# Optimization experiments

Hardware: AMD Instinct MI355X
Metric: run time of the kernel (lower is better)

## Reference

```python
import jax, jax.numpy as jnp
from jax import lax
import numpy as np

D_MODEL = 1024
D_STATE = 16
D_CONV = 4
EXPAND = 2
D_INNER = EXPAND * D_MODEL  # 2048
DT_RANK = D_MODEL // 16     # 64
BATCH = 2
SEQLEN = 1024


def setup_inputs() -> dict:
    key = jax.random.key(0)
    ks = iter(jax.random.split(key, 32))

    def nrm(shape, s=0.02):
        return jax.random.normal(next(ks), shape, jnp.float32) * s

    def mamba_params():
        return dict(
            Win=nrm((2 * D_INNER, D_MODEL)), bin=jnp.zeros((2 * D_INNER,), jnp.float32),
            convw=nrm((D_INNER, D_CONV), 0.1), convb=jnp.zeros((D_INNER,), jnp.float32),
            Wx=nrm((DT_RANK + 2 * D_STATE, D_INNER)),
            Wdt=nrm((D_INNER, DT_RANK), 0.1), bdt=nrm((D_INNER,), 0.1),
            Alog=jnp.log(jnp.broadcast_to(jnp.arange(1, D_STATE + 1, dtype=jnp.float32), (D_INNER, D_STATE))),
            Dsk=jnp.ones((D_INNER,), jnp.float32),
            Wout=nrm((D_MODEL, D_INNER)), bout=jnp.zeros((D_MODEL,), jnp.float32),
        )

    inp = {"x": jax.random.normal(next(ks), (BATCH, SEQLEN, D_MODEL), jnp.float32)}
    for pref, p in (("f_", mamba_params()), ("b_", mamba_params())):
        for k, v in p.items():
            inp[pref + k] = v
    inp["proj_W"] = nrm((D_MODEL, 2 * D_MODEL))
    inp["proj_b"] = jnp.zeros((D_MODEL,), jnp.float32)
    return inp


def selective_scan(u, delta, A, Bm, Cm, Dsk):
    # u, delta: (B,L,Di); Bm, Cm: (B,L,N); A: (Di,N); Dsk: (Di,)
    def step(h, inp):
        u_t, d_t, b_t, c_t = inp  # (B,Di),(B,Di),(B,N),(B,N)
        dA = jnp.exp(d_t[..., None] * A)                      # (B,Di,N)
        h = h * dA + (d_t * u_t)[..., None] * b_t[:, None, :]  # (B,Di,N)
        y = jnp.einsum('bdn,bn->bd', h, c_t)
        return h, y

    h0 = jnp.zeros((u.shape[0], A.shape[0], A.shape[1]), u.dtype)
    xs = (u.transpose(1, 0, 2), delta.transpose(1, 0, 2),
          Bm.transpose(1, 0, 2), Cm.transpose(1, 0, 2))
    _, ys = lax.scan(step, h0, xs)
    return ys.transpose(1, 0, 2) + u * Dsk  # (B,L,Di)


def mamba_fwd(x, Win, bin_, convw, convb, Wx, Wdt, bdt, Alog, Dsk, Wout, bout):
    xz = x @ Win.T + bin_                      # (B,L,2*Di)
    xin, z = jnp.split(xz, 2, axis=-1)
    # causal depthwise conv over time: (B,Di,L)
    xc = lax.conv_general_dilated(
        xin.transpose(0, 2, 1), convw[:, None, :], (1,), [(D_CONV - 1, 0)],
        dimension_numbers=('NCH', 'OIH', 'NCH'), feature_group_count=D_INNER)
    u = jax.nn.silu(xc.transpose(0, 2, 1) + convb)  # (B,L,Di)
    xdbl = u @ Wx.T                                 # (B,L,dt_rank+2N)
    dt, Bm, Cm = jnp.split(xdbl, [DT_RANK, DT_RANK + D_STATE], axis=-1)
    delta = jax.nn.softplus(dt @ Wdt.T + bdt)       # (B,L,Di)
    A = -jnp.exp(Alog)
    y = selective_scan(u, delta, A, Bm, Cm, Dsk)
    y = y * jax.nn.silu(z)
    return y @ Wout.T + bout


def reference(x,
              f_Win, f_bin, f_convw, f_convb, f_Wx, f_Wdt, f_bdt, f_Alog, f_Dsk, f_Wout, f_bout,
              b_Win, b_bin, b_convw, b_convb, b_Wx, b_Wdt, b_bdt, b_Alog, b_Dsk, b_Wout, b_bout,
              proj_W, proj_b):
    out_f = mamba_fwd(x, f_Win, f_bin, f_convw, f_convb, f_Wx, f_Wdt, f_bdt, f_Alog, f_Dsk, f_Wout, f_bout)
    xr = jnp.flip(x, axis=1)
    out_b = mamba_fwd(xr, b_Win, b_bin, b_convw, b_convb, b_Wx, b_Wdt, b_bdt, b_Alog, b_Dsk, b_Wout, b_bout)
    out_b = jnp.flip(out_b, axis=1)
    out = jnp.concatenate([out_f, out_b], axis=-1)  # (B,L,2*d_model)
    return out @ proj_W.T + proj_b
```

## Files before the change

kernel.cpp:

```cpp
#include <hip/hip_runtime.h>
#include <math.h>

#define D_MODEL 1024
#define D_STATE 16
#define D_CONV  4
#define D_INNER 2048
#define DT_RANK 64
#define BATCH   2
#define SEQLEN  1024
#define MROWS   2048
#define XDBL_LD 128
#define NCHUNK  32
#define CLEN    (SEQLEN / NCHUNK)
#define NCHG    8192

typedef __attribute__((ext_vector_type(8))) short bf16x8;
typedef __attribute__((ext_vector_type(4))) float f32x4;

#define BARR() asm volatile("s_barrier" ::: "memory")
#define VMW(n) asm volatile("s_waitcnt vmcnt(" #n ")" ::: "memory")
#define LGKM(n) asm volatile("s_waitcnt lgkmcnt(" #n ")" ::: "memory")
#define SCHB() __builtin_amdgcn_sched_barrier(0)

static __device__ __forceinline__ float sigmoidf_(float x) {
    return 1.f / (1.f + __expf(-x));
}
static __device__ __forceinline__ unsigned short bf16rn(float f) {
    unsigned u = __float_as_uint(f);
    return (unsigned short)((u + 0x7FFFu + ((u >> 16) & 1u)) >> 16);
}
static __device__ __forceinline__ void hl_split(float f, unsigned short& h, unsigned short& l) {
    h = bf16rn(f);
    l = bf16rn(f - __uint_as_float((unsigned)h << 16));
}
static __device__ __forceinline__ float us2f(unsigned short u) {
    return __uint_as_float((unsigned)u << 16);
}

static __device__ __forceinline__
void split_block(const float* __restrict__ in, int R, int C, int ldin,
                 unsigned short* __restrict__ out, int Rout, bool flip,
                 int blk, int tid)
{
    int q = blk * 256 + tid;
    int qpr = C >> 2;
    int row = q / qpr;
    int c4 = (q - row * qpr) << 2;
    if (row >= Rout) return;
    unsigned short h[4] = {0, 0, 0, 0}, l[4] = {0, 0, 0, 0};
    if (row < R) {
        int sr = row;
        if (flip) { int b = row >> 10, t = row & 1023; sr = (b << 10) + (1023 - t); }
        float4 v = *(const float4*)(in + (size_t)sr * ldin + c4);
        float f[4] = {v.x, v.y, v.z, v.w};
        #pragma unroll
        for (int i = 0; i < 4; ++i) hl_split(f[i], h[i], l[i]);
    }
    size_t ob = (size_t)row * (2 * C);
    *(ushort4*)(out + ob + c4)     = make_ushort4(h[0], h[1], h[2], h[3]);
    *(ushort4*)(out + ob + C + c4) = make_ushort4(l[0], l[1], l[2], l[3]);
}

__global__ __launch_bounds__(256)
void prep1_kernel(const float* __restrict__ x,
                  const float* __restrict__ Win0, const float* __restrict__ Win1,
                  const float* __restrict__ Wx0,  const float* __restrict__ Wx1,
                  const float* __restrict__ Wdt0, const float* __restrict__ Wdt1,
                  unsigned short* xc0,
                  unsigned short* Winb0, unsigned short* Winb1,
                  unsigned short* Wxb0, unsigned short* Wxb1,
                  unsigned short* Wdtb0, unsigned short* Wdtb1)
{
    int b = blockIdx.x, tid = threadIdx.x;
    if      (b < 2048)  split_block(x,    MROWS, D_MODEL, D_MODEL, xc0,  MROWS, false, b,        tid);
    else if (b < 6144)  split_block(Win0, 4096,  D_MODEL, D_MODEL, Winb0, 4096, false, b - 2048, tid);
    else if (b < 10240) split_block(Win1, 4096,  D_MODEL, D_MODEL, Winb1, 4096, false, b - 6144, tid);
    else if (b < 10496) split_block(Wx0,  96,    D_INNER, D_INNER, Wxb0,  128,  false, b - 10240, tid);
    else if (b < 10752) split_block(Wx1,  96,    D_INNER, D_INNER, Wxb1,  128,  false, b - 10496, tid);
    else if (b < 10880) split_block(Wdt0, D_INNER, DT_RANK, DT_RANK, Wdtb0, D_INNER, false, b - 10752, tid);
    else                split_block(Wdt1, D_INNER, DT_RANK, DT_RANK, Wdtb1, D_INNER, false, b - 10880, tid);
}

#define SWZ(row) (((row) >> 1) & 3)
#define RDA(p, kk, row) (*(const bf16x8*)&AS[p][kk][row][(fs ^ SWZ(row)) << 3])
#define RDB(p, kk, row) (*(const bf16x8*)&BS[p][kk][row][(fs ^ SWZ(row)) << 3])

#define MFMA16(ACCBASE, AF, BF) \
    _Pragma("unroll") for (int f = 0; f < 4; ++f) \
    _Pragma("unroll") for (int g = 0; g < 4; ++g) \
        acc[(ACCBASE) + f][g] = __builtin_amdgcn_mfma_f32_16x16x32_bf16(AF[f], BF[g], acc[(ACCBASE) + f][g], 0, 0, 0);

#define KTILE(MODE, kt) do { \
    const int p_ = (kt) & 1; \
    const int pn_ = ((kt) + 1) & 1; \
    {  \
        if (MODE < 2) stageA((kt) + 1, 1); \
        BARR(); \
        _Pragma("unroll") for (int f = 0; f < 4; ++f) { int rw = wm + 64 + f * 16 + fr; aFB[f] = RDA(p_, 0, rw); } \
        LGKM(4); SCHB(); \
        __builtin_amdgcn_s_setprio(1); \
        MFMA16(0, aFA, bFA) \
        __builtin_amdgcn_s_setprio(0); \
    } \
    {  \
        if (MODE == 0) stageB((kt) + 2, 0); \
        BARR(); \
        _Pragma("unroll") for (int f = 0; f < 4; ++f) { int rw = wm + f * 16 + fr; aFA[f] = RDA(p_, 1, rw); } \
        _Pragma("unroll") for (int g = 0; g < 4; ++g) { int rw = wn + g * 16 + fr; bFB[g] = RDB(p_, 1, rw); } \
        LGKM(8); SCHB(); \
        __builtin_amdgcn_s_setprio(1); \
        MFMA16(4, aFB, bFA) \
        __builtin_amdgcn_s_setprio(0); \
    } \
    {  \
        if (MODE == 0) stageA((kt) + 2, 0); \
        BARR(); \
        _Pragma("unroll") for (int f = 0; f < 4; ++f) { int rw = wm + 64 + f * 16 + fr; aFB[f] = RDA(p_, 1, rw); } \
        LGKM(4); SCHB(); \
        __builtin_amdgcn_s_setprio(1); \
        MFMA16(0, aFA, bFB) \
        __builtin_amdgcn_s_setprio(0); \
    } \
    {  \
        if (MODE == 0) { VMW(4); } else if (MODE == 1) { VMW(0); } \
        if (MODE == 0) stageB((kt) + 2, 1); \
        BARR(); \
        if (MODE < 2) { \
            _Pragma("unroll") for (int f = 0; f < 4; ++f) { int rw = wm + f * 16 + fr; aFA[f] = RDA(pn_, 0, rw); } \
            _Pragma("unroll") for (int g = 0; g < 4; ++g) { int rw = wn + g * 16 + fr; bFA[g] = RDB(pn_, 0, rw); } \
            LGKM(8); \
        } else { LGKM(0); } \
        SCHB(); \
        __builtin_amdgcn_s_setprio(1); \
        MFMA16(4, aFB, bFB) \
        __builtin_amdgcn_s_setprio(0); \
    } \
} while (0)

template<int ACT, bool PART, int KTS, bool DUALN, int SEGS>
__global__ __launch_bounds__(512, 1)
void gemm256(const unsigned short* __restrict__ A0,
             const unsigned short* __restrict__ A1,
             const unsigned short* __restrict__ W0,
             const unsigned short* __restrict__ W1,
             const float* __restrict__ bias0,
             const float* __restrict__ bias1,
             float* __restrict__ C0, float* __restrict__ C1,
             float* __restrict__ part,
             int ldc, int N, int K, int nks)
{
    __shared__ unsigned short AS[2][2][256][32];
    __shared__ unsigned short BS[2][2][256][32];

    const int tid = threadIdx.x;
    const int lane = tid & 63;
    const int wid = tid >> 6;

    const int z = blockIdx.z;
    const int zdir = z / nks;
    const int ks = z - zdir * nks;

    const int nbx = gridDim.x;
    const int nby = gridDim.y;
    const int nwg = nbx * nby;
    int bid = blockIdx.y * nbx + blockIdx.x;
    int q8 = nwg >> 3;
    int swz = (bid & 7) * q8 + (bid >> 3);
    const int bm = (swz % nby) * 256;
    const int bn = (swz / nby) * 256;

    int dn, bnn;
    if (DUALN) { dn = (bn >= (N >> 1)) ? 1 : 0; bnn = bn - dn * (N >> 1); }
    else       { dn = zdir; bnn = bn; }
    const unsigned short* A = (DUALN || dn == 0) ? A0 : A1;
    const unsigned short* W = dn ? W1 : W0;

    const int ldg = 2 * K;
    constexpr int NT = SEGS * KTS;
    const int Kc = KTS * 64;
    const int kbase = ks * Kc;

    const int wm = (wid >> 2) * 128;
    const int wn = (wid & 3) * 64;
    const int fr = lane & 15;
    const int fs = lane >> 4;

    f32x4 acc[8][4];
    #pragma unroll
    for (int i = 0; i < 8; ++i)
        #pragma unroll
        for (int j = 0; j < 4; ++j) {
            f32x4 zv = {0.f, 0.f, 0.f, 0.f};
            acc[i][j] = zv;
        }

    auto koffA = [&](int t) { unsigned tu = (unsigned)t; unsigned sg = tu / KTS;
                              unsigned w = tu - sg * KTS;
                              return (int)((sg == 1 ? (unsigned)K : 0u) + kbase + w * 64); };
    auto koffB = [&](int t) { unsigned tu = (unsigned)t; unsigned sg = tu / KTS;
                              unsigned w = tu - sg * KTS;
                              return (int)((sg == 2 ? (unsigned)K : 0u) + kbase + w * 64); };

    auto stageA = [&](int t, int kk) {
        int ko = koffA(t) + kk * 32;
        unsigned short* dst = &AS[t & 1][kk][0][0];
        #pragma unroll
        for (int i = 0; i < 2; ++i) {
            int s = i * 512 + tid;
            int row = s >> 2, sl = s & 3, lsl = sl ^ SWZ(row);
            const unsigned short* src = A + (size_t)(bm + row) * ldg + ko + lsl * 8;
            __builtin_amdgcn_global_load_lds(
                (const __attribute__((address_space(1))) void*)src,
                (__attribute__((address_space(3))) void*)(dst + s * 8), 16, 0, 0);
        }
    };
    auto stageB = [&](int t, int kk) {
        int ko = koffB(t) + kk * 32;
        unsigned short* dst = &BS[t & 1][kk][0][0];
        #pragma unroll
        for (int i = 0; i < 2; ++i) {
            int s = i * 512 + tid;
            int row = s >> 2, sl = s & 3, lsl = sl ^ SWZ(row);
            const unsigned short* src = W + (size_t)(bnn + row) * ldg + ko + lsl * 8;
            __builtin_amdgcn_global_load_lds(
                (const __attribute__((address_space(1))) void*)src,
                (__attribute__((address_space(3))) void*)(dst + s * 8), 16, 0, 0);
        }
    };

    stageB(0, 0); stageA(0, 0); stageB(0, 1); stageA(0, 1);
    stageB(1, 0); stageA(1, 0); stageB(1, 1);
    VMW(6);
    BARR();

    bf16x8 aFA[4], aFB[4], bFA[4], bFB[4];
    #pragma unroll
    for (int f = 0; f < 4; ++f) { int rw = wm + f * 16 + fr; aFA[f] = RDA(0, 0, rw); }
    #pragma unroll
    for (int g = 0; g < 4; ++g) { int rw = wn + g * 16 + fr; bFA[g] = RDB(0, 0, rw); }

    #pragma unroll 1
    for (int kt = 0; kt < NT - 2; ++kt) KTILE(0, kt);
    KTILE(1, NT - 2);
    KTILE(2, NT - 1);

    if (PART) {
        float* P = part + (size_t)z * ((size_t)MROWS * N);
        #pragma unroll
        for (int i = 0; i < 8; ++i)
            #pragma unroll
            for (int j = 0; j < 4; ++j) {
                int coln = bnn + wn + j * 16 + fr;
                #pragma unroll
                for (int r = 0; r < 4; ++r) {
                    int rowm = bm + wm + i * 16 + fs * 4 + r;
                    P[(size_t)rowm * N + coln] = acc[i][j][r];
                }
            }
    } else {
        const float* bias = dn ? bias1 : bias0;
        float* C = dn ? C1 : C0;
        #pragma unroll
        for (int i = 0; i < 8; ++i)
            #pragma unroll
            for (int j = 0; j < 4; ++j) {
                int coln = bnn + wn + j * 16 + fr;
                float bv = bias ? bias[coln] : 0.f;
                #pragma unroll
                for (int r = 0; r < 4; ++r) {
                    int rowm = bm + wm + i * 16 + fs * 4 + r;
                    float v = acc[i][j][r] + bv;
                    if (ACT == 1) v = (v > 20.f) ? v : log1pf(__expf(v));
                    int crow = rowm;
                    if (DUALN && dn) { int bb = rowm >> 10, t = rowm & 1023; crow = (bb << 10) + 1023 - t; }
                    C[(size_t)crow * ldc + coln] = v;
                }
            }
    }
}

template<int ACT, bool PART>
__global__ __launch_bounds__(256)
void gemm_mfma(const unsigned short* __restrict__ A0,
               const unsigned short* __restrict__ A1,
               const unsigned short* __restrict__ W0,
               const unsigned short* __restrict__ W1,
               const float* __restrict__ bias0,
               const float* __restrict__ bias1,
               float* __restrict__ C0, float* __restrict__ C1,
               float* __restrict__ part,
               int ldc, int N, int K, int nks)
{
    __shared__ __align__(16) unsigned short As[128 * 32];
    __shared__ __align__(16) unsigned short Bs[128 * 32];

    const int tid = threadIdx.x;
    const int lane = tid & 63;
    const int wid = tid >> 6;

    const int z = blockIdx.z;
    const int dir = z / nks;
    const int ks = z - dir * nks;
    const unsigned short* A = dir ? A1 : A0;
    const unsigned short* W = dir ? W1 : W0;

    const int nbx = gridDim.x;
    const int nwg = nbx * gridDim.y;
    int bid = blockIdx.y * nbx + blockIdx.x;
    int q8 = nwg >> 3;
    int swz = (nwg >= 8) ? (bid & 7) * q8 + (bid >> 3) : bid;
    const int bm = (swz / nbx) * 128;
    const int bn = (swz % nbx) * 128;

    const int ldg = 2 * K;
    const int Kc = K / nks;
    const int kbase = ks * Kc;

    f32x4 acc[4][4];
    #pragma unroll
    for (int i = 0; i < 4; ++i)
        #pragma unroll
        for (int j = 0; j < 4; ++j) {
            f32x4 zv = {0.f, 0.f, 0.f, 0.f};
            acc[i][j] = zv;
        }

    const int r0 = tid >> 2;
    const int k0s = (tid & 3) ^ ((r0 >> 1) & 3);
    const int r1 = (256 + tid) >> 2;
    const int k1s = (tid & 3) ^ ((r1 >> 1) & 3);

    unsigned short* As_w0 = &As[(wid << 6) * 8];
    unsigned short* As_w1 = &As[(256 + (wid << 6)) * 8];
    unsigned short* Bs_w0 = &Bs[(wid << 6) * 8];
    unsigned short* Bs_w1 = &Bs[(256 + (wid << 6)) * 8];

    const int wm = (wid >> 1) * 64;
    const int wn = (wid & 1) * 64;
    const int fr = lane & 15;
    const int fs = lane >> 4;

    const int KS = Kc >> 5;
    #pragma unroll 1
    for (int seg = 0; seg < 3; ++seg) {
        const int aoff = ((seg == 1) ? K : 0) + kbase;
        const int boff = ((seg == 2) ? K : 0) + kbase;
        #pragma unroll 1
        for (int kt = 0; kt < KS; ++kt) {
            const int kk = kt << 5;
            const unsigned short* ga0 = A + (size_t)(bm + r0) * ldg + aoff + kk + k0s * 8;
            const unsigned short* ga1 = A + (size_t)(bm + r1) * ldg + aoff + kk + k1s * 8;
            const unsigned short* gw0 = W + (size_t)(bn + r0) * ldg + boff + kk + k0s * 8;
            const unsigned short* gw1 = W + (size_t)(bn + r1) * ldg + boff + kk + k1s * 8;
            __builtin_amdgcn_global_load_lds(
                (const __attribute__((address_space(1))) void*)ga0,
                (__attribute__((address_space(3))) void*)As_w0, 16, 0, 0);
            __builtin_amdgcn_global_load_lds(
                (const __attribute__((address_space(1))) void*)ga1,
                (__attribute__((address_space(3))) void*)As_w1, 16, 0, 0);
            __builtin_amdgcn_global_load_lds(
                (const __attribute__((address_space(1))) void*)gw0,
                (__attribute__((address_space(3))) void*)Bs_w0, 16, 0, 0);
            __builtin_amdgcn_global_load_lds(
                (const __attribute__((address_space(1))) void*)gw1,
                (__attribute__((address_space(3))) void*)Bs_w1, 16, 0, 0);
            __syncthreads();

            bf16x8 aF[4], bF[4];
            #pragma unroll
            for (int f = 0; f < 4; ++f) {
                int ra = wm + f * 16 + fr;
                int sa = fs ^ ((ra >> 1) & 3);
                aF[f] = *(const bf16x8*)&As[ra * 32 + sa * 8];
                int rb = wn + f * 16 + fr;
                int sb = fs ^ ((rb >> 1) & 3);
                bF[f] = *(const bf16x8*)&Bs[rb * 32 + sb * 8];
            }
            #pragma unroll
            for (int i = 0; i < 4; ++i)
                #pragma unroll
                for (int j = 0; j < 4; ++j)
                    acc[i][j] = __builtin_amdgcn_mfma_f32_16x16x32_bf16(
                        aF[i], bF[j], acc[i][j], 0, 0, 0);
            __syncthreads();
        }
    }

    if (PART) {
        float* P = part + (size_t)z * ((size_t)MROWS * N);
        #pragma unroll
        for (int i = 0; i < 4; ++i)
            #pragma unroll
            for (int j = 0; j < 4; ++j) {
                int coln = bn + wn + j * 16 + fr;
                #pragma unroll
                for (int r = 0; r < 4; ++r) {
                    int rowm = bm + wm + i * 16 + fs * 4 + r;
                    P[(size_t)rowm * N + coln] = acc[i][j][r];
                }
            }
    } else {
        const float* bias = dir ? bias1 : bias0;
        float* C = dir ? C1 : C0;
        #pragma unroll
        for (int i = 0; i < 4; ++i)
            #pragma unroll
            for (int j = 0; j < 4; ++j) {
                int coln = bn + wn + j * 16 + fr;
                float bv = bias ? bias[coln] : 0.f;
                #pragma unroll
                for (int r = 0; r < 4; ++r) {
                    int rowm = bm + wm + i * 16 + fs * 4 + r;
                    float v = acc[i][j][r] + bv;
                    if (ACT == 1) v = (v > 20.f) ? v : log1pf(__expf(v));
                    C[(size_t)rowm * ldc + coln] = v;
                }
            }
    }
}

__global__ __launch_bounds__(256)
void reduce_xdbl_k(const float* __restrict__ part,
                   float* __restrict__ xdbl0, float* __restrict__ xdbl1,
                   unsigned short* __restrict__ dtb0, unsigned short* __restrict__ dtb1)
{
    const int dz = blockIdx.z;
    const float* P = part + (size_t)dz * 16 * MROWS * XDBL_LD;
    float* xdbl = dz ? xdbl1 : xdbl0;
    unsigned short* dtb = dz ? dtb1 : dtb0;
    int i = blockIdx.x * 256 + threadIdx.x;
    int row = i >> 5;
    int c4 = (i & 31) << 2;
    float4 s = make_float4(0.f, 0.f, 0.f, 0.f);
    #pragma unroll
    for (int k = 0; k < 16; ++k) {
        float4 v = *(const float4*)(P + (size_t)k * MROWS * XDBL_LD + (size_t)row * XDBL_LD + c4);
        s.x += v.x; s.y += v.y; s.z += v.z; s.w += v.w;
    }
    *(float4*)(xdbl + (size_t)row * XDBL_LD + c4) = s;
    if (c4 < DT_RANK) {
        float f[4] = {s.x, s.y, s.z, s.w};
        unsigned short h[4], l[4];
        #pragma unroll
        for (int j = 0; j < 4; ++j) hl_split(f[j], h[j], l[j]);
        *(ushort4*)(dtb + (size_t)row * (2 * DT_RANK) + c4) = make_ushort4(h[0], h[1], h[2], h[3]);
        *(ushort4*)(dtb + (size_t)row * (2 * DT_RANK) + DT_RANK + c4) = make_ushort4(l[0], l[1], l[2], l[3]);
    }
}

__global__ __launch_bounds__(256)
void mid_kernel(const float* __restrict__ part2,
                const float* __restrict__ bout0, const float* __restrict__ bout1,
                unsigned short* __restrict__ tmpb,
                const float* __restrict__ projW, unsigned short* __restrict__ pWb)
{
    const int dz = blockIdx.z;
    const int tid = threadIdx.x;
    if (dz == 2) {
        split_block(projW, D_MODEL, 2 * D_MODEL, 2 * D_MODEL, pWb, D_MODEL, false, blockIdx.x, tid);
        return;
    }
    const float* P = part2 + (size_t)dz * 4 * MROWS * D_MODEL;
    const float* bias = dz ? bout1 : bout0;
    const int colofs = dz ? D_MODEL : 0;
    int i = blockIdx.x * 256 + tid;
    int row = i >> 8;
    int c4 = (i & 255) << 2;
    float4 s = make_float4(bias[c4], bias[c4 + 1], bias[c4 + 2], bias[c4 + 3]);
    #pragma unroll
    for (int k = 0; k < 4; ++k) {
        float4 v = *(const float4*)(P + (size_t)k * MROWS * D_MODEL + (size_t)row * D_MODEL + c4);
        s.x += v.x; s.y += v.y; s.z += v.z; s.w += v.w;
    }
    int orow = row;
    if (dz) { int bb = row >> 10, t = row & 1023; orow = (bb << 10) + 1023 - t; }
    float f[4] = {s.x, s.y, s.z, s.w};
    unsigned short h[4], l[4];
    #pragma unroll
    for (int j = 0; j < 4; ++j) hl_split(f[j], h[j], l[j]);
    *(ushort4*)(tmpb + (size_t)orow * 4096 + colofs + c4) = make_ushort4(h[0], h[1], h[2], h[3]);
    *(ushort4*)(tmpb + (size_t)orow * 4096 + 2048 + colofs + c4) = make_ushort4(l[0], l[1], l[2], l[3]);
}

__global__ __launch_bounds__(256)
void reduce_out_k(const float* __restrict__ part, const float* __restrict__ bias,
                  float* __restrict__ out)
{
    int i = blockIdx.x * 256 + threadIdx.x;
    int row = i >> 8;
    int c4 = (i & 255) << 2;
    float4 s = make_float4(bias[c4], bias[c4 + 1], bias[c4 + 2], bias[c4 + 3]);
    #pragma unroll
    for (int k = 0; k < 8; ++k) {
        float4 v = *(const float4*)(part + (size_t)k * MROWS * D_MODEL + (size_t)row * D_MODEL + c4);
        s.x += v.x; s.y += v.y; s.z += v.z; s.w += v.w;
    }
    *(float4*)(out + (size_t)row * D_MODEL + c4) = s;
}

__global__ __launch_bounds__(256)
void conv_prep_kernel(const float* __restrict__ xz0, const float* __restrict__ xz1,
                      const float* __restrict__ cw0, const float* __restrict__ cw1,
                      const float* __restrict__ cb0, const float* __restrict__ cb1,
                      unsigned short* __restrict__ ub0, unsigned short* __restrict__ ub1,
                      const float* __restrict__ Wout0, const float* __restrict__ Wout1,
                      unsigned short* __restrict__ Woutb0, unsigned short* __restrict__ Woutb1)
{
    const int dz = blockIdx.z;
    const int tid = threadIdx.x;
    if (dz == 2) {
        int b = blockIdx.x;
        if (b < 2048) split_block(Wout0, D_MODEL, D_INNER, D_INNER, Woutb0, D_MODEL, false, b, tid);
        else if (b < 4096) split_block(Wout1, D_MODEL, D_INNER, D_INNER, Woutb1, D_MODEL, false, b - 2048, tid);
        return;
    }
    const float* xz = dz ? xz1 : xz0;
    const float* convw = dz ? cw1 : cw0;
    const float* convb = dz ? cb1 : cb0;
    unsigned short* ub = dz ? ub1 : ub0;
    int idx = blockIdx.x * 256 + tid;
    int d = idx % D_INNER;
    int r = idx / D_INNER;
    int t = r % SEQLEN;
    float acc = convb[d];
    #pragma unroll
    for (int k = 0; k < D_CONV; ++k) {
        int back = D_CONV - 1 - k;
        if (t - back >= 0)
            acc += xz[(size_t)(r - back) * (2 * D_INNER) + d] * convw[d * D_CONV + k];
    }
    float v = acc * sigmoidf_(acc);
    unsigned short h, l;
    hl_split(v, h, l);
    ub[(size_t)r * (2 * D_INNER) + d] = h;
    ub[(size_t)r * (2 * D_INNER) + D_INNER + d] = l;
}

__global__ __launch_bounds__(256)
void scan_phase1(const float* __restrict__ delta0, const float* __restrict__ delta1,
                 const unsigned short* __restrict__ ub0, const unsigned short* __restrict__ ub1,
                 const float* __restrict__ xdbl0, const float* __restrict__ xdbl1,
                 const float* __restrict__ Alog0, const float* __restrict__ Alog1,
                 float* __restrict__ aprod, float* __restrict__ hfin)
{
    const int gid = blockIdx.x * 256 + threadIdx.x;
    const int chg = gid & (NCHG - 1);
    const int chunk = gid >> 13;
    const int dir = chg >> 12;
    const int bd = chg & 4095;
    const int b = bd >> 11, d = bd & 2047;
    const float* delta = dir ? delta1 : delta0;
    const unsigned short* ub = dir ? ub1 : ub0;
    const float* xdbl = dir ? xdbl1 : xdbl0;
    const float* Alog = dir ? Alog1 : Alog0;

    float Av[16], h[16], ap[16];
    #pragma unroll
    for (int n = 0; n < 16; ++n) {
        Av[n] = -__expf(Alog[d * D_STATE + n]);
        h[n] = 0.f; ap[n] = 1.f;
    }
    const int t0 = chunk * CLEN;
    for (int t = t0; t < t0 + CLEN; ++t) {
        const size_t r = (size_t)b * SEQLEN + t;
        float dlt = delta[r * D_INNER + d];
        float uu = us2f(ub[r * 4096 + d]) + us2f(ub[r * 4096 + 2048 + d]);
        float du = dlt * uu;
        float4 bq[4];
        #pragma unroll
        for (int q = 0; q < 4; ++q)
            bq[q] = *(const float4*)(xdbl + r * XDBL_LD + DT_RANK + q * 4);
        #pragma unroll
        for (int n = 0; n < 16; ++n) {
            float Bv = ((const float*)&bq[n >> 2])[n & 3];
            float dA = __expf(dlt * Av[n]);
            h[n] = h[n] * dA + du * Bv;
            ap[n] *= dA;
        }
    }
    float* pa = aprod + (size_t)chunk * (NCHG * 16) + (size_t)chg * 16;
    float* pf = hfin  + (size_t)chunk * (NCHG * 16) + (size_t)chg * 16;
    #pragma unroll
    for (int q = 0; q < 4; ++q) {
        *(float4*)(pa + q * 4) = make_float4(ap[q*4], ap[q*4+1], ap[q*4+2], ap[q*4+3]);
        *(float4*)(pf + q * 4) = make_float4(h[q*4], h[q*4+1], h[q*4+2], h[q*4+3]);
    }
}

__global__ __launch_bounds__(256)
void scan_phase2(float* __restrict__ aprod ,
                 const float* __restrict__ hfin)
{
    const int gid = blockIdx.x * 256 + threadIdx.x;
    float h = 0.f;
    for (int c = 0; c < NCHUNK; ++c) {
        const size_t idx = (size_t)c * (NCHG * 16) + gid;
        float a = aprod[idx];
        float f = hfin[idx];
        aprod[idx] = h;
        h = a * h + f;
    }
}

__global__ __launch_bounds__(256)
void scan_phase3(const float* __restrict__ delta0, const float* __restrict__ delta1,
                 unsigned short* __restrict__ ub0, unsigned short* __restrict__ ub1,
                 const float* __restrict__ xdbl0, const float* __restrict__ xdbl1,
                 const float* __restrict__ Alog0, const float* __restrict__ Alog1,
                 const float* __restrict__ Dsk0, const float* __restrict__ Dsk1,
                 const float* __restrict__ xz0, const float* __restrict__ xz1,
                 const float* __restrict__ hin)
{
    const int gid = blockIdx.x * 256 + threadIdx.x;
    const int chg = gid & (NCHG - 1);
    const int chunk = gid >> 13;
    const int dir = chg >> 12;
    const int bd = chg & 4095;
    const int b = bd >> 11, d = bd & 2047;
    const float* delta = dir ? delta1 : delta0;
    unsigned short* ub = dir ? ub1 : ub0;
    const float* xdbl = dir ? xdbl1 : xdbl0;
    const float* Alog = dir ? Alog1 : Alog0;
    const float* Dsk = dir ? Dsk1 : Dsk0;
    const float* xz = dir ? xz1 : xz0;

    float Av[16], h[16];
    const float* ph = hin + (size_t)chunk * (NCHG * 16) + (size_t)chg * 16;
    #pragma unroll
    for (int n = 0; n < 16; ++n) {
        Av[n] = -__expf(Alog[d * D_STATE + n]);
        h[n] = ph[n];
    }
    const float Dv = Dsk[d];
    const int t0 = chunk * CLEN;
    for (int t = t0; t < t0 + CLEN; ++t) {
        const size_t r = (size_t)b * SEQLEN + t;
        float dlt = delta[r * D_INNER + d];
        float uu = us2f(ub[r * 4096 + d]) + us2f(ub[r * 4096 + 2048 + d]);
        float du = dlt * uu;
        float4 bq[4], cq[4];
        #pragma unroll
        for (int q = 0; q < 4; ++q) {
            bq[q] = *(const float4*)(xdbl + r * XDBL_LD + DT_RANK + q * 4);
            cq[q] = *(const float4*)(xdbl + r * XDBL_LD + DT_RANK + D_STATE + q * 4);
        }
        float p0 = 0.f, p1 = 0.f, p2 = 0.f, p3 = 0.f;
        #pragma unroll
        for (int n = 0; n < 16; ++n) {
            float Bv = ((const float*)&bq[n >> 2])[n & 3];
            float Cv = ((const float*)&cq[n >> 2])[n & 3];
            float dA = __expf(dlt * Av[n]);
            h[n] = h[n] * dA + du * Bv;
            if ((n & 3) == 0) p0 += h[n] * Cv;
            else if ((n & 3) == 1) p1 += h[n] * Cv;
            else if ((n & 3) == 2) p2 += h[n] * Cv;
            else p3 += h[n] * Cv;
        }
        float y = ((p0 + p1) + (p2 + p3)) + uu * Dv;
        float zv = xz[r * (2 * D_INNER) + D_INNER + d];
        float v = y * (zv * sigmoidf_(zv));
        unsigned short hh, ll;
        hl_split(v, hh, ll);
        ub[r * 4096 + d] = hh;
        ub[r * 4096 + 2048 + d] = ll;
    }
}

extern "C" void kernel_launch(void* const* d_in, const int* in_sizes, int n_in,
                              void* d_out, int out_size, void* d_ws, size_t ws_size,
                              hipStream_t stream)
{
    const float* x = (const float*)d_in[0];
    const float* proj_W = (const float*)d_in[23];
    const float* proj_b = (const float*)d_in[24];
    float* out = (float*)d_out;

    const float *Win[2], *bin_[2], *convw[2], *convb[2], *Wx[2], *Wdt[2], *bdt[2],
                *Alog[2], *Dsk[2], *Wout[2], *bout[2];
    for (int dir = 0; dir < 2; ++dir) {
        const int base = 1 + dir * 11;
        Win[dir]   = (const float*)d_in[base + 0];
        bin_[dir]  = (const float*)d_in[base + 1];
        convw[dir] = (const float*)d_in[base + 2];
        convb[dir] = (const float*)d_in[base + 3];
        Wx[dir]    = (const float*)d_in[base + 4];
        Wdt[dir]   = (const float*)d_in[base + 5];
        bdt[dir]   = (const float*)d_in[base + 6];
        Alog[dir]  = (const float*)d_in[base + 7];
        Dsk[dir]   = (const float*)d_in[base + 8];
        Wout[dir]  = (const float*)d_in[base + 9];
        bout[dir]  = (const float*)d_in[base + 10];
    }

    char* ws = (char*)d_ws;
    const size_t MB = 1ull << 20;
    float* xz[2]            = {(float*)(ws + 0 * MB),   (float*)(ws + 32 * MB)};
    unsigned short* ub[2]   = {(unsigned short*)(ws + 64 * MB),
                               (unsigned short*)(ws + 80 * MB)};
    unsigned short* Winb[2] = {(unsigned short*)(ws + 96 * MB),
                               (unsigned short*)(ws + 112 * MB)};
    unsigned short* xc0     = (unsigned short*)(ws + 128 * MB);
    float* part             = (float*)(ws + 112 * MB);
    float* part2            = (float*)(ws + 0 * MB);
    float* delta[2]         = {(float*)(ws + 112 * MB), (float*)(ws + 128 * MB)};
    unsigned short* Woutb[2]= {(unsigned short*)(ws + 96 * MB),
                               (unsigned short*)(ws + 104 * MB)};
    unsigned short* yzb[2]  = {ub[0], ub[1]};
    unsigned short* tmpb    = ub[0];
    unsigned short* pWb     = ub[1];
    unsigned short* Wxb[2]  = {(unsigned short*)(ws + 144 * MB), (unsigned short*)(ws + 145 * MB)};
    unsigned short* Wdtb[2] = {(unsigned short*)(ws + 146 * MB), (unsigned short*)(ws + 146 * MB + 512 * 1024)};
    unsigned short* dtb[2]  = {(unsigned short*)(ws + 147 * MB), (unsigned short*)(ws + 147 * MB + 512 * 1024)};
    float* xdbl[2]          = {(float*)(ws + 148 * MB), (float*)(ws + 149 * MB)};
    float* aprod            = (float*)(ws + 150 * MB);
    float* hfin             = (float*)(ws + 167 * MB);

    dim3 blk(256);

    prep1_kernel<<<11008, blk, 0, stream>>>(
        x, Win[0], Win[1], Wx[0], Wx[1], Wdt[0], Wdt[1],
        xc0, Winb[0], Winb[1], Wxb[0], Wxb[1], Wdtb[0], Wdtb[1]);

    gemm256<0, false, 16, true, 2><<<dim3(32, 8, 1), dim3(512), 0, stream>>>(
        xc0, nullptr, Winb[0], Winb[1], bin_[0], bin_[1], xz[0], xz[1],
        nullptr, 4096, 8192, D_MODEL, 1);

    conv_prep_kernel<<<dim3((MROWS * D_INNER) / 256, 1, 3), blk, 0, stream>>>(
        xz[0], xz[1], convw[0], convw[1], convb[0], convb[1], ub[0], ub[1],
        Wout[0], Wout[1], Woutb[0], Woutb[1]);

    gemm_mfma<0, true><<<dim3(1, 16, 32), blk, 0, stream>>>(
        ub[0], ub[1], Wxb[0], Wxb[1], nullptr, nullptr, nullptr, nullptr,
        part, XDBL_LD, XDBL_LD, D_INNER, 16);

    reduce_xdbl_k<<<dim3(256, 1, 2), blk, 0, stream>>>(
        part, xdbl[0], xdbl[1], dtb[0], dtb[1]);

    gemm_mfma<1, false><<<dim3(16, 16, 2), blk, 0, stream>>>(
        dtb[0], dtb[1], Wdtb[0], Wdtb[1], bdt[0], bdt[1], delta[0], delta[1],
        nullptr, D_INNER, D_INNER, DT_RANK, 1);

    scan_phase1<<<NCHUNK * NCHG / 256, blk, 0, stream>>>(
        delta[0], delta[1], ub[0], ub[1], xdbl[0], xdbl[1], Alog[0], Alog[1],
        aprod, hfin);
    scan_phase2<<<NCHG * 16 / 256, blk, 0, stream>>>(aprod, hfin);
    scan_phase3<<<NCHUNK * NCHG / 256, blk, 0, stream>>>(
        delta[0], delta[1], ub[0], ub[1], xdbl[0], xdbl[1], Alog[0], Alog[1],
        Dsk[0], Dsk[1], xz[0], xz[1], aprod);

    gemm256<0, true, 8, false, 2><<<dim3(4, 8, 8), dim3(512), 0, stream>>>(
        yzb[0], yzb[1], Woutb[0], Woutb[1], nullptr, nullptr, nullptr, nullptr,
        part2, D_MODEL, D_MODEL, D_INNER, 4);

    mid_kernel<<<dim3(2048, 1, 3), blk, 0, stream>>>(
        part2, bout[0], bout[1], tmpb, proj_W, pWb);

    gemm256<0, true, 4, false, 2><<<dim3(4, 8, 8), dim3(512), 0, stream>>>(
        tmpb, nullptr, pWb, nullptr, nullptr, nullptr, nullptr, nullptr,
        part2, D_MODEL, D_MODEL, 2 * D_MODEL, 8);

    reduce_out_k<<<2048, blk, 0, stream>>>(part2, proj_b, out);
}
```

Before: 402.7 us.

## Replace split-K output GEMMs with 128-tile GEMMs fusing bias and split epilogues

The Wout and final projection GEMMs switch from 256-tile split-K kernels that write fp32 partials (reduced by mid_kernel and reduce_out_k) to a new 128x128-tile GEMM. That GEMM runs the full K loop and applies bias, the flip and the bf16 hi/lo split, or writes the final output, in its epilogue. This drops two reduction kernels and the partial-buffer traffic, at the cost of fewer, longer workgroups with no K parallelism. Weight splitting also stops writing the low bf16 half for Win, Wout and proj_W, which cuts write traffic but only works if the GEMMs read just the high half of those weights.

```diff
diff --git a/kernel.cpp b/kernel.cpp
--- a/kernel.cpp
+++ b/kernel.cpp
@@ -40,7 +40,7 @@
 static __device__ __forceinline__
 void split_block(const float* __restrict__ in, int R, int C, int ldin,
                  unsigned short* __restrict__ out, int Rout, bool flip,
-                 int blk, int tid)
+                 int blk, int tid, bool wlo)
 {
     int q = blk * 256 + tid;
     int qpr = C >> 2;
@@ -57,8 +57,9 @@
         for (int i = 0; i < 4; ++i) hl_split(f[i], h[i], l[i]);
     }
     size_t ob = (size_t)row * (2 * C);
-    *(ushort4*)(out + ob + c4)     = make_ushort4(h[0], h[1], h[2], h[3]);
-    *(ushort4*)(out + ob + C + c4) = make_ushort4(l[0], l[1], l[2], l[3]);
+    *(ushort4*)(out + ob + c4) = make_ushort4(h[0], h[1], h[2], h[3]);
+    if (wlo)
+        *(ushort4*)(out + ob + C + c4) = make_ushort4(l[0], l[1], l[2], l[3]);
 }
 
 __global__ __launch_bounds__(256)
@@ -72,13 +73,13 @@
                   unsigned short* Wdtb0, unsigned short* Wdtb1)
 {
     int b = blockIdx.x, tid = threadIdx.x;
-    if      (b < 2048)  split_block(x,    MROWS, D_MODEL, D_MODEL, xc0,  MROWS, false, b,        tid);
-    else if (b < 6144)  split_block(Win0, 4096,  D_MODEL, D_MODEL, Winb0, 4096, false, b - 2048, tid);
-    else if (b < 10240) split_block(Win1, 4096,  D_MODEL, D_MODEL, Winb1, 4096, false, b - 6144, tid);
-    else if (b < 10496) split_block(Wx0,  96,    D_INNER, D_INNER, Wxb0,  128,  false, b - 10240, tid);
-    else if (b < 10752) split_block(Wx1,  96,    D_INNER, D_INNER, Wxb1,  128,  false, b - 10496, tid);
-    else if (b < 10880) split_block(Wdt0, D_INNER, DT_RANK, DT_RANK, Wdtb0, D_INNER, false, b - 10752, tid);
-    else                split_block(Wdt1, D_INNER, DT_RANK, DT_RANK, Wdtb1, D_INNER, false, b - 10880, tid);
+    if      (b < 2048)  split_block(x,    MROWS, D_MODEL, D_MODEL, xc0,  MROWS, false, b,        tid, true);
+    else if (b < 6144)  split_block(Win0, 4096,  D_MODEL, D_MODEL, Winb0, 4096, false, b - 2048, tid, false);
+    else if (b < 10240) split_block(Win1, 4096,  D_MODEL, D_MODEL, Winb1, 4096, false, b - 6144, tid, false);
+    else if (b < 10496) split_block(Wx0,  96,    D_INNER, D_INNER, Wxb0,  128,  false, b - 10240, tid, true);
+    else if (b < 10752) split_block(Wx1,  96,    D_INNER, D_INNER, Wxb1,  128,  false, b - 10496, tid, true);
+    else if (b < 10880) split_block(Wdt0, D_INNER, DT_RANK, DT_RANK, Wdtb0, D_INNER, false, b - 10752, tid, true);
+    else                split_block(Wdt1, D_INNER, DT_RANK, DT_RANK, Wdtb1, D_INNER, false, b - 10880, tid, true);
 }
 
 #define SWZ(row) (((row) >> 1) & 3)
@@ -137,7 +138,7 @@
     } \
 } while (0)
 
-template<int ACT, bool PART, int KTS, bool DUALN, int SEGS>
+template<int KTS, bool DUALN, int SEGS>
 __global__ __launch_bounds__(512, 1)
 void gemm256(const unsigned short* __restrict__ A0,
              const unsigned short* __restrict__ A1,
@@ -146,8 +147,7 @@
              const float* __restrict__ bias0,
              const float* __restrict__ bias1,
              float* __restrict__ C0, float* __restrict__ C1,
-             float* __restrict__ part,
-             int ldc, int N, int K, int nks)
+             int ldc, int N, int K)
 {
     __shared__ unsigned short AS[2][2][256][32];
     __shared__ unsigned short BS[2][2][256][32];
@@ -156,9 +156,7 @@
     const int lane = tid & 63;
     const int wid = tid >> 6;
 
-    const int z = blockIdx.z;
-    const int zdir = z / nks;
-    const int ks = z - zdir * nks;
+    const int zdir = blockIdx.z;
 
     const int nbx = gridDim.x;
     const int nby = gridDim.y;
@@ -177,8 +175,6 @@
 
     const int ldg = 2 * K;
     constexpr int NT = SEGS * KTS;
-    const int Kc = KTS * 64;
-    const int kbase = ks * Kc;
 
     const int wm = (wid >> 2) * 128;
     const int wn = (wid & 3) * 64;
@@ -196,10 +192,10 @@
 
     auto koffA = [&](int t) { unsigned tu = (unsigned)t; unsigned sg = tu / KTS;
                               unsigned w = tu - sg * KTS;
-                              return (int)((sg == 1 ? (unsigned)K : 0u) + kbase + w * 64); };
+                              return (int)((sg == 1 ? (unsigned)K : 0u) + w * 64); };
     auto koffB = [&](int t) { unsigned tu = (unsigned)t; unsigned sg = tu / KTS;
                               unsigned w = tu - sg * KTS;
-                              return (int)((sg == 2 ? (unsigned)K : 0u) + kbase + w * 64); };
+                              return (int)((sg == 2 ? (unsigned)K : 0u) + w * 64); };
 
     auto stageA = [&](int t, int kk) {
         int ko = koffA(t) + kk * 32;
@@ -244,36 +240,187 @@
     KTILE(1, NT - 2);
     KTILE(2, NT - 1);
 
-    if (PART) {
-        float* P = part + (size_t)z * ((size_t)MROWS * N);
-        #pragma unroll
-        for (int i = 0; i < 8; ++i)
+    const float* bias = dn ? bias1 : bias0;
+    float* C = dn ? C1 : C0;
+    #pragma unroll
+    for (int i = 0; i < 8; ++i)
+        #pragma unroll
+        for (int j = 0; j < 4; ++j) {
+            int coln = bnn + wn + j * 16 + fr;
+            float bv = bias ? bias[coln] : 0.f;
+            #pragma unroll
+            for (int r = 0; r < 4; ++r) {
+                int rowm = bm + wm + i * 16 + fs * 4 + r;
+                float v = acc[i][j][r] + bv;
+                int crow = rowm;
+                if (DUALN && dn) { int bb = rowm >> 10, t = rowm & 1023; crow = (bb << 10) + 1023 - t; }
+                C[(size_t)crow * ldc + coln] = v;
+            }
+        }
+}
+
+#define MF16(AF, BF) \
+    _Pragma("unroll") for (int f = 0; f < 4; ++f) \
+    _Pragma("unroll") for (int g = 0; g < 4; ++g) \
+        acc[f][g] = __builtin_amdgcn_mfma_f32_16x16x32_bf16(AF[f], BF[g], acc[f][g], 0, 0, 0);
+
+#define KT128(MODE, kt) do { \
+    const int p_ = (kt) & 1; \
+    const int pn_ = ((kt) + 1) & 1; \
+    {  \
+        if (MODE == 0) { stageA((kt) + 1, 0); stageB((kt) + 1, 0); VMW(4); } \
+        else { VMW(0); } \
+        BARR(); \
+        _Pragma("unroll") for (int f = 0; f < 4; ++f) { int rw = wm + f * 16 + fr; aFB[f] = RDA(p_, 1, rw); } \
+        _Pragma("unroll") for (int g = 0; g < 4; ++g) { int rw = wn + g * 16 + fr; bFB[g] = RDB(p_, 1, rw); } \
+        LGKM(8); SCHB(); \
+        __builtin_amdgcn_s_setprio(1); \
+        MF16(aFA, bFA) \
+        __builtin_amdgcn_s_setprio(0); \
+    } \
+    {  \
+        if (MODE == 0) { \
+            stageA((kt) + 1, 1); stageB((kt) + 1, 1); VMW(4); BARR(); \
+            _Pragma("unroll") for (int f = 0; f < 4; ++f) { int rw = wm + f * 16 + fr; aFA[f] = RDA(pn_, 0, rw); } \
+            _Pragma("unroll") for (int g = 0; g < 4; ++g) { int rw = wn + g * 16 + fr; bFA[g] = RDB(pn_, 0, rw); } \
+            LGKM(8); \
+        } else { LGKM(0); } \
+        SCHB(); \
+        __builtin_amdgcn_s_setprio(1); \
+        MF16(aFB, bFB) \
+        __builtin_amdgcn_s_setprio(0); \
+    } \
+} while (0)
+
+template<int EPI, int KTS, int SEGS>
+__global__ __launch_bounds__(256, 2)
+void gemm128p(const unsigned short* __restrict__ A0,
+              const unsigned short* __restrict__ A1,
+              const unsigned short* __restrict__ W0,
+              const unsigned short* __restrict__ W1,
+              const float* __restrict__ bias0,
+              const float* __restrict__ bias1,
+              float* __restrict__ C0f,
+              unsigned short* __restrict__ Tb,
+              int ldc, int K)
+{
+    __shared__ unsigned short AS[2][2][128][32];
+    __shared__ unsigned short BS[2][2][128][32];
+
+    const int tid = threadIdx.x;
+    const int lane = tid & 63;
+    const int wid = tid >> 6;
+
+    const int dir = blockIdx.z;
+    const unsigned short* A = dir ? A1 : A0;
+    const unsigned short* W = dir ? W1 : W0;
+
+    const int nbx = gridDim.x;
+    const int nwg = nbx * gridDim.y;
+    int bid = blockIdx.y * nbx + blockIdx.x;
+    int q8 = nwg >> 3;
+    int swz = (bid & 7) * q8 + (bid >> 3);
+    const int bm = (swz / nbx) * 128;
+    const int bn = (swz % nbx) * 128;
+
+    const int ldg = 2 * K;
+    constexpr int NT = SEGS * KTS;
+
+    const int wm = (wid >> 1) * 64;
+    const int wn = (wid & 1) * 64;
+    const int fr = lane & 15;
+    const int fs = lane >> 4;
+
+    f32x4 acc[4][4];
+    #pragma unroll
+    for (int i = 0; i < 4; ++i)
+        #pragma unroll
+        for (int j = 0; j < 4; ++j) {
+            f32x4 zv = {0.f, 0.f, 0.f, 0.f};
+            acc[i][j] = zv;
+        }
+
+    auto koffA = [&](int t) { unsigned tu = (unsigned)t; unsigned sg = tu / KTS;
+                              unsigned w = tu - sg * KTS;
+                              return (int)((sg == 1 ? (unsigned)K : 0u) + w * 64); };
+    auto koffB = [&](int t) { unsigned tu = (unsigned)t; unsigned sg = tu / KTS;
+                              unsigned w = tu - sg * KTS;
+                              return (int)((sg == 2 ? (unsigned)K : 0u) + w * 64); };
+
+    auto stageA = [&](int t, int kk) {
+        int ko = koffA(t) + kk * 32;
+        unsigned short* dst = &AS[t & 1][kk][0][0];
+        #pragma unroll
+        for (int i = 0; i < 2; ++i) {
+            int s = i * 256 + tid;
+            int row = s >> 2, sl = s & 3, lsl = sl ^ SWZ(row);
+            const unsigned short* src = A + (size_t)(bm + row) * ldg + ko + lsl * 8;
+            __builtin_amdgcn_global_load_lds(
+                (const __attribute__((address_space(1))) void*)src,
+                (__attribute__((address_space(3))) void*)(dst + s * 8), 16, 0, 0);
+        }
+    };
+    auto stageB = [&](int t, int kk) {
+        int ko = koffB(t) + kk * 32;
+        unsigned short* dst = &BS[t & 1][kk][0][0];
+        #pragma unroll
+        for (int i = 0; i < 2; ++i) {
+            int s = i * 256 + tid;
+            int row = s >> 2, sl = s & 3, lsl = sl ^ SWZ(row);
+            const unsigned short* src = W + (size_t)(bn + row) * ldg + ko + lsl * 8;
+            __builtin_amdgcn_global_load_lds(
+                (const __attribute__((address_space(1))) void*)src,
+                (__attribute__((address_space(3))) void*)(dst + s * 8), 16, 0, 0);
+        }
+    };
+
+    stageA(0, 0); stageB(0, 0); stageA(0, 1); stageB(0, 1);
+    VMW(4);
+    BARR();
+
+    bf16x8 aFA[4], aFB[4], bFA[4], bFB[4];
+    #pragma unroll
+    for (int f = 0; f < 4; ++f) { int rw = wm + f * 16 + fr; aFA[f] = RDA(0, 0, rw); }
+    #pragma unroll
+    for (int g = 0; g < 4; ++g) { int rw = wn + g * 16 + fr; bFA[g] = RDB(0, 0, rw); }
+
+    #pragma unroll 1
+    for (int kt = 0; kt < NT - 1; ++kt) KT128(0, kt);
+    KT128(2, NT - 1);
+
+    const float* bias = dir ? bias1 : bias0;
+    if (EPI == 0) {
+        float* C = C0f;
+        #pragma unroll
+        for (int i = 0; i < 4; ++i)
             #pragma unroll
             for (int j = 0; j < 4; ++j) {
-                int coln = bnn + wn + j * 16 + fr;
-                #pragma unroll
-                for (int r = 0; r < 4; ++r) {
-                    int rowm = bm + wm + i * 16 + fs * 4 + r;
-                    P[(size_t)rowm * N + coln] = acc[i][j][r];
-                }
-            }
-    } else {
-        const float* bias = dn ? bias1 : bias0;
-        float* C = dn ? C1 : C0;
-        #pragma unroll
-        for (int i = 0; i < 8; ++i)
-            #pragma unroll
-            for (int j = 0; j < 4; ++j) {
-                int coln = bnn + wn + j * 16 + fr;
+                int coln = bn + wn + j * 16 + fr;
                 float bv = bias ? bias[coln] : 0.f;
                 #pragma unroll
                 for (int r = 0; r < 4; ++r) {
                     int rowm = bm + wm + i * 16 + fs * 4 + r;
+                    C[(size_t)rowm * ldc + coln] = acc[i][j][r] + bv;
+                }
+            }
+    } else {
+        const int colofs = dir ? D_MODEL : 0;
+        #pragma unroll
+        for (int i = 0; i < 4; ++i)
+            #pragma unroll
+            for (int j = 0; j < 4; ++j) {
+                int coln = bn + wn + j * 16 + fr;
+                float bv = bias[coln];
+                #pragma unroll
+                for (int r = 0; r < 4; ++r) {
+                    int rowm = bm + wm + i * 16 + fs * 4 + r;
                     float v = acc[i][j][r] + bv;
-                    if (ACT == 1) v = (v > 20.f) ? v : log1pf(__expf(v));
-                    int crow = rowm;
-                    if (DUALN && dn) { int bb = rowm >> 10, t = rowm & 1023; crow = (bb << 10) + 1023 - t; }
-                    C[(size_t)crow * ldc + coln] = v;
+                    int orow = rowm;
+                    if (dir) { int bb = rowm >> 10, t = rowm & 1023; orow = (bb << 10) + 1023 - t; }
+                    unsigned short h, l;
+                    hl_split(v, h, l);
+                    Tb[(size_t)orow * 4096 + colofs + coln] = h;
+                    Tb[(size_t)orow * 4096 + 2048 + colofs + coln] = l;
                 }
             }
     }
@@ -449,53 +596,10 @@
 }
 
 __global__ __launch_bounds__(256)
-void mid_kernel(const float* __restrict__ part2,
-                const float* __restrict__ bout0, const float* __restrict__ bout1,
-                unsigned short* __restrict__ tmpb,
-                const float* __restrict__ projW, unsigned short* __restrict__ pWb)
-{
-    const int dz = blockIdx.z;
-    const int tid = threadIdx.x;
-    if (dz == 2) {
-        split_block(projW, D_MODEL, 2 * D_MODEL, 2 * D_MODEL, pWb, D_MODEL, false, blockIdx.x, tid);
-        return;
-    }
-    const float* P = part2 + (size_t)dz * 4 * MROWS * D_MODEL;
-    const float* bias = dz ? bout1 : bout0;
-    const int colofs = dz ? D_MODEL : 0;
-    int i = blockIdx.x * 256 + tid;
-    int row = i >> 8;
-    int c4 = (i & 255) << 2;
-    float4 s = make_float4(bias[c4], bias[c4 + 1], bias[c4 + 2], bias[c4 + 3]);
-    #pragma unroll
-    for (int k = 0; k < 4; ++k) {
-        float4 v = *(const float4*)(P + (size_t)k * MROWS * D_MODEL + (size_t)row * D_MODEL + c4);
-        s.x += v.x; s.y += v.y; s.z += v.z; s.w += v.w;
-    }
-    int orow = row;
-    if (dz) { int bb = row >> 10, t = row & 1023; orow = (bb << 10) + 1023 - t; }
-    float f[4] = {s.x, s.y, s.z, s.w};
-    unsigned short h[4], l[4];
-    #pragma unroll
-    for (int j = 0; j < 4; ++j) hl_split(f[j], h[j], l[j]);
-    *(ushort4*)(tmpb + (size_t)orow * 4096 + colofs + c4) = make_ushort4(h[0], h[1], h[2], h[3]);
-    *(ushort4*)(tmpb + (size_t)orow * 4096 + 2048 + colofs + c4) = make_ushort4(l[0], l[1], l[2], l[3]);
-}
-
-__global__ __launch_bounds__(256)
-void reduce_out_k(const float* __restrict__ part, const float* __restrict__ bias,
-                  float* __restrict__ out)
-{
-    int i = blockIdx.x * 256 + threadIdx.x;
-    int row = i >> 8;
-    int c4 = (i & 255) << 2;
-    float4 s = make_float4(bias[c4], bias[c4 + 1], bias[c4 + 2], bias[c4 + 3]);
-    #pragma unroll
-    for (int k = 0; k < 8; ++k) {
-        float4 v = *(const float4*)(part + (size_t)k * MROWS * D_MODEL + (size_t)row * D_MODEL + c4);
-        s.x += v.x; s.y += v.y; s.z += v.z; s.w += v.w;
-    }
-    *(float4*)(out + (size_t)row * D_MODEL + c4) = s;
+void pwsplit_kernel(const float* __restrict__ projW, unsigned short* __restrict__ pWb)
+{
+    split_block(projW, D_MODEL, 2 * D_MODEL, 2 * D_MODEL, pWb, D_MODEL, false,
+                blockIdx.x, threadIdx.x, false);
 }
 
 __global__ __launch_bounds__(256)
@@ -510,8 +614,8 @@
     const int tid = threadIdx.x;
     if (dz == 2) {
         int b = blockIdx.x;
-        if (b < 2048) split_block(Wout0, D_MODEL, D_INNER, D_INNER, Woutb0, D_MODEL, false, b, tid);
-        else if (b < 4096) split_block(Wout1, D_MODEL, D_INNER, D_INNER, Woutb1, D_MODEL, false, b - 2048, tid);
+        if (b < 2048) split_block(Wout0, D_MODEL, D_INNER, D_INNER, Woutb0, D_MODEL, false, b, tid, false);
+        else if (b < 4096) split_block(Wout1, D_MODEL, D_INNER, D_INNER, Woutb1, D_MODEL, false, b - 2048, tid, false);
         return;
     }
     const float* xz = dz ? xz1 : xz0;
@@ -701,12 +805,11 @@
                                (unsigned short*)(ws + 112 * MB)};
     unsigned short* xc0     = (unsigned short*)(ws + 128 * MB);
     float* part             = (float*)(ws + 112 * MB);
-    float* part2            = (float*)(ws + 0 * MB);
     float* delta[2]         = {(float*)(ws + 112 * MB), (float*)(ws + 128 * MB)};
     unsigned short* Woutb[2]= {(unsigned short*)(ws + 96 * MB),
                                (unsigned short*)(ws + 104 * MB)};
     unsigned short* yzb[2]  = {ub[0], ub[1]};
-    unsigned short* tmpb    = ub[0];
+    unsigned short* tmpb    = (unsigned short*)(ws + 0 * MB);
     unsigned short* pWb     = ub[1];
     unsigned short* Wxb[2]  = {(unsigned short*)(ws + 144 * MB), (unsigned short*)(ws + 145 * MB)};
     unsigned short* Wdtb[2] = {(unsigned short*)(ws + 146 * MB), (unsigned short*)(ws + 146 * MB + 512 * 1024)};
@@ -721,9 +824,9 @@
         x, Win[0], Win[1], Wx[0], Wx[1], Wdt[0], Wdt[1],
         xc0, Winb[0], Winb[1], Wxb[0], Wxb[1], Wdtb[0], Wdtb[1]);
 
-    gemm256<0, false, 16, true, 2><<<dim3(32, 8, 1), dim3(512), 0, stream>>>(
+    gemm256<16, true, 2><<<dim3(32, 8, 1), dim3(512), 0, stream>>>(
         xc0, nullptr, Winb[0], Winb[1], bin_[0], bin_[1], xz[0], xz[1],
-        nullptr, 4096, 8192, D_MODEL, 1);
+        4096, 8192, D_MODEL);
 
     conv_prep_kernel<<<dim3((MROWS * D_INNER) / 256, 1, 3), blk, 0, stream>>>(
         xz[0], xz[1], convw[0], convw[1], convb[0], convb[1], ub[0], ub[1],
@@ -748,16 +851,13 @@
         delta[0], delta[1], ub[0], ub[1], xdbl[0], xdbl[1], Alog[0], Alog[1],
         Dsk[0], Dsk[1], xz[0], xz[1], aprod);
 
-    gemm256<0, true, 8, false, 2><<<dim3(4, 8, 8), dim3(512), 0, stream>>>(
-        yzb[0], yzb[1], Woutb[0], Woutb[1], nullptr, nullptr, nullptr, nullptr,
-        part2, D_MODEL, D_MODEL, D_INNER, 4);
-
-    mid_kernel<<<dim3(2048, 1, 3), blk, 0, stream>>>(
-        part2, bout[0], bout[1], tmpb, proj_W, pWb);
-
-    gemm256<0, true, 4, false, 2><<<dim3(4, 8, 8), dim3(512), 0, stream>>>(
-        tmpb, nullptr, pWb, nullptr, nullptr, nullptr, nullptr, nullptr,
-        part2, D_MODEL, D_MODEL, 2 * D_MODEL, 8);
-
-    reduce_out_k<<<2048, blk, 0, stream>>>(part2, proj_b, out);
-}
+    gemm128p<2, 32, 2><<<dim3(8, 16, 2), blk, 0, stream>>>(
+        yzb[0], yzb[1], Woutb[0], Woutb[1], bout[0], bout[1],
+        nullptr, tmpb, 0, D_INNER);
+
+    pwsplit_kernel<<<2048, blk, 0, stream>>>(proj_W, pWb);
+
+    gemm128p<0, 32, 2><<<dim3(8, 16, 1), blk, 0, stream>>>(
+        tmpb, nullptr, pWb, nullptr, proj_b, nullptr,
+        out, nullptr, D_MODEL, 2 * D_MODEL);
+}
```

After: 429.8 us. 6.7% more time.
